# Kernel optimization log

Measured on AMD Instinct MI355X. Metric: run time of the kernel, lower is better.

## Reference

```python
import jax, jax.numpy as jnp
import numpy as np

# --- dims (match init_kwargs) ---
B, IN_DIM, OUT_DIM, CAUSES_DIM = 4096, 512, 4096, 256
POOL = 2
N_STEPS = 10
GAMMA = 0.1
LR = 0.001  # fixed lr inside _IstaStep
S = int(np.sqrt(OUT_DIM))   # 64: side of the square code map
SP = S // POOL              # 32: pooled side
POOLED_DIM = SP * SP        # 1024: second dim of V (pool path)


def setup_inputs() -> dict:
    key = jax.random.key(0)
    k1, k2, k3 = jax.random.split(key, 3)
    inputs = jax.random.normal(k1, (B, IN_DIM), jnp.float32)
    limit = float(np.sqrt(6.0 / (OUT_DIM + IN_DIM)))  # glorot_uniform for W
    W = jax.random.uniform(k2, (OUT_DIM, IN_DIM), jnp.float32, -limit, limit)
    # pool_flag=True -> V ~ U(0, 1) with shape (causes_dim, pooled_dim)
    V = jax.random.uniform(k3, (CAUSES_DIM, POOLED_DIM), jnp.float32, 0.0, 1.0)
    return {"inputs": inputs, "W": W, "V": V}


def _soft_threshold(x, t):
    # _proxOp: max(x - t, 0) + min(x + t, 0)
    return jnp.maximum(x - t, 0.0) + jnp.minimum(x + t, 0.0)


def reference(inputs, W, V):
    Bn = inputs.shape[0]
    x0 = jnp.zeros((Bn, OUT_DIM), inputs.dtype)
    u0 = jnp.full((Bn, CAUSES_DIM), 0.1, inputs.dtype)   # zeros + 0.1
    rec0 = jnp.zeros((Bn, IN_DIM), inputs.dtype)

    def step(carry, _):
        x, u, _rec = carry
        outputs = x @ W                                   # [B, IN_DIM], linear activation
        # NOTE: original uses (1 + exp(-z)) * 0.5 (not a true sigmoid) — keep faithful
        causes = (1.0 + jnp.exp(-(u @ V))) * 0.5          # [B, POOLED_DIM]
        # nearest-neighbor upsample of the pooled cause map back to the code map
        causes_up = jnp.repeat(
            jnp.repeat(causes.reshape(Bn, SP, SP), POOL, axis=1), POOL, axis=2
        ).reshape(Bn, OUT_DIM)                            # [B, OUT_DIM]
        # T.grad(sum((inputs - x@W)^2), x) = 2 * (x@W - inputs) @ W.T
        grad_x = 2.0 * (outputs - inputs) @ W.T           # [B, OUT_DIM]
        # prior=0 in _get_output, so the _proxInnov branch is dead code
        x_new = jax.lax.stop_gradient(                    # disconnected_grad
            _soft_threshold(x - LR * grad_x, LR * GAMMA * causes_up))
        # 2x2 max pool over the square code map
        x_pool = x_new.reshape(Bn, SP, POOL, SP, POOL).max(axis=(2, 4)).reshape(Bn, POOLED_DIM)
        # T.grad(sum(causes(u) * x_pool * gamma), u): d causes/dz = -0.5*exp(-z)
        dcauses = -0.5 * jnp.exp(-(u @ V))                # [B, POOLED_DIM]
        grad_u = (dcauses * x_pool * GAMMA) @ V.T         # [B, CAUSES_DIM]
        u_new = jax.lax.stop_gradient(
            _soft_threshold(u - LR * grad_u, LR * GAMMA / 10.0))
        return (x_new, u_new, outputs), None

    (x, u, rec), _ = jax.lax.scan(step, (x0, u0, rec0), None, length=N_STEPS)
    # return_mode='rec': reconstruction computed in the last step (from x_{T-1})
    return rec
```

## Files before the change

kernel.cpp:

```cpp
#include <hip/hip_runtime.h>
#include <math.h>


#define NB 4096
#define IN_DIM 512
#define OUT_DIM 4096
#define CAUSES_DIM 256
#define POOLED_DIM 1024

typedef __attribute__((ext_vector_type(8))) short short8;
typedef __attribute__((ext_vector_type(4))) float f32x4;

static constexpr float LR = 0.001f;
static constexpr float GAMMA = 0.1f;

enum { EP_R = 0, EP_OUT, EP_UUP };

__device__ __forceinline__ float softthr(float v, float t) {
    return fmaxf(v - t, 0.0f) + fminf(v + t, 0.0f);
}
__device__ __forceinline__ unsigned short f2bf(float f) {
    unsigned int u = __builtin_bit_cast(unsigned int, f);
    u = (u + 0x7fffu + ((u >> 16) & 1u)) >> 16;
    return (unsigned short)u;
}
__device__ __forceinline__ float bf2f(unsigned short h) {
    return __builtin_bit_cast(float, (unsigned int)h << 16);
}
__device__ __forceinline__ void gload_lds16(const unsigned short* g, unsigned short* l) {
    __builtin_amdgcn_global_load_lds(
        (const __attribute__((address_space(1))) void*)g,
        (__attribute__((address_space(3))) void*)l, 16, 0, 0);
}

template<int ROWS, int K>
__device__ __forceinline__ void stage_tile(const unsigned short* __restrict__ g,
                                           unsigned short* l, int row0, int k0, int t)
{
#pragma unroll
    for (int j = 0; j < ROWS / 32; j++) {
        const int idx = j * 256 + t;
        const int row = idx >> 3;
        const int sl  = (idx & 7) ^ (row & 7);
        gload_lds16(g + (size_t)(row0 + row) * K + k0 + sl * 8,
                    l + (size_t)(idx & ~63) * 8);
    }
}

template<int BM, int BN, int N, int K, int EP>
__device__ void gemm_core(unsigned short* lds, int bid,
                          const unsigned short* __restrict__ A,
                          const unsigned short* __restrict__ B,
                          const float* __restrict__ auxf,
                          void* __restrict__ out0, void* __restrict__ out1)
{
    constexpr int WM = BM / 2, WN = BN / 2;
    constexpr int FM = WM / 16, FN = WN / 16;
    constexpr int NK = K / 64, NX = N / BN;
    constexpr int NWG = (NB / BM) * NX;
    constexpr int TILE = (BM + BN) * 64;
    unsigned short* A0 = lds;
    unsigned short* B0 = lds + BM * 64;
    unsigned short* A1 = lds + TILE;
    unsigned short* B1 = lds + TILE + BM * 64;

    const int t    = threadIdx.x;
    const int lane = t & 63, wid = t >> 6;
    const int l15  = lane & 15, l7 = lane & 7, g = lane >> 4;
    const int work = ((bid & 7) * (NWG / 8)) + (bid >> 3);
    const int bn = work % NX, bm = work / NX;
    const int m0 = bm * BM, n0 = bn * BN;
    const int wm0 = (wid >> 1) * WM, wn0 = (wid & 1) * WN;

    f32x4 acc[FM][FN];
#pragma unroll
    for (int fi = 0; fi < FM; fi++)
#pragma unroll
        for (int fj = 0; fj < FN; fj++) acc[fi][fj] = (f32x4){0.f, 0.f, 0.f, 0.f};

    auto compute = [&](const unsigned short* As, const unsigned short* Bs) {
#pragma unroll
        for (int ks = 0; ks < 2; ks++) {
            const int so = (((ks * 4) + g) ^ l7) * 8;
            short8 af[FM], bfv[FN];
#pragma unroll
            for (int fi = 0; fi < FM; fi++)
                af[fi] = *(const short8*)&As[(wm0 + fi * 16 + l15) * 64 + so];
#pragma unroll
            for (int fj = 0; fj < FN; fj++)
                bfv[fj] = *(const short8*)&Bs[(wn0 + fj * 16 + l15) * 64 + so];
#pragma unroll
            for (int fi = 0; fi < FM; fi++)
#pragma unroll
                for (int fj = 0; fj < FN; fj++)
                    acc[fi][fj] = __builtin_amdgcn_mfma_f32_16x16x32_bf16(
                        af[fi], bfv[fj], acc[fi][fj], 0, 0, 0);
        }
    };

    stage_tile<BM, K>(A, A0, m0, 0, t);
    stage_tile<BN, K>(B, B0, n0, 0, t);
    __syncthreads();
#pragma unroll 1
    for (int kt = 0; kt < NK; kt += 2) {
        stage_tile<BM, K>(A, A1, m0, (kt + 1) * 64, t);
        stage_tile<BN, K>(B, B1, n0, (kt + 1) * 64, t);
        compute(A0, B0);
        __syncthreads();
        if (kt + 2 < NK) {
            stage_tile<BM, K>(A, A0, m0, (kt + 2) * 64, t);
            stage_tile<BN, K>(B, B0, n0, (kt + 2) * 64, t);
        }
        compute(A1, B1);
        __syncthreads();
    }

#pragma unroll
    for (int fi = 0; fi < FM; fi++) {
#pragma unroll
        for (int fj = 0; fj < FN; fj++) {
#pragma unroll
            for (int r = 0; r < 4; r++) {
                const int row = m0 + wm0 + fi * 16 + g * 4 + r;
                const int col = n0 + wn0 + fj * 16 + l15;
                const float v = acc[fi][fj][r];
                if (EP == EP_R) {
                    ((unsigned short*)out0)[(size_t)row * N + col] =
                        f2bf(v - auxf[(size_t)row * N + col]);
                } else if (EP == EP_OUT) {
                    ((float*)out0)[(size_t)row * N + col] = v;
                } else {
                    float* up = (float*)out0;
                    const size_t idx = (size_t)row * CAUSES_DIM + col;
                    const float uv = softthr(up[idx] - LR * v, LR * GAMMA * 0.1f);
                    up[idx] = uv;
                    ((unsigned short*)out1)[idx] = f2bf(uv);
                }
            }
        }
    }
}

template<bool POOLF>
__global__ __launch_bounds__(256)
void xupc_kernel(const unsigned short* __restrict__ Rbf,
                 const unsigned short* __restrict__ Wbf,
                 const unsigned short* __restrict__ ubf,
                 const unsigned short* __restrict__ VTbf,
                 unsigned short* __restrict__ xbf,
                 unsigned short* __restrict__ gbf)
{
    constexpr int BM = 128, BN = 128, K = IN_DIM, NK = K / 64;
    constexpr int NX = OUT_DIM / BN, NWG = (NB / BM) * NX;
    constexpr int TILE = (BM + BN) * 64;
    __shared__ unsigned short lds[2 * TILE];
    unsigned short* A0 = lds;
    unsigned short* B0 = lds + BM * 64;
    unsigned short* A1 = lds + TILE;
    unsigned short* B1 = lds + TILE + BM * 64;
    unsigned* czdc = (unsigned*)(lds + 2 * TILE - 8192);
    unsigned short* xs = lds;

    const int t    = threadIdx.x;
    const int lane = t & 63, wid = t >> 6;
    const int l15  = lane & 15, l7 = lane & 7, g = lane >> 4;
    const int work = ((blockIdx.x & 7) * (NWG / 8)) + (blockIdx.x >> 3);
    const int bn = work % NX, bm = work / NX;
    const int m0 = bm * BM, n0 = bn * BN;
    const int wm0 = (wid >> 1) * 64, wn0 = (wid & 1) * 64;

    f32x4 acc[4][4];
#pragma unroll
    for (int fi = 0; fi < 4; fi++)
#pragma unroll
        for (int fj = 0; fj < 4; fj++) acc[fi][fj] = (f32x4){0.f, 0.f, 0.f, 0.f};

    auto compute = [&](const unsigned short* As, const unsigned short* Bs) {
#pragma unroll
        for (int ks = 0; ks < 2; ks++) {
            const int so = (((ks * 4) + g) ^ l7) * 8;
            short8 af[4], bfv[4];
#pragma unroll
            for (int fi = 0; fi < 4; fi++)
                af[fi] = *(const short8*)&As[(wm0 + fi * 16 + l15) * 64 + so];
#pragma unroll
            for (int fj = 0; fj < 4; fj++)
                bfv[fj] = *(const short8*)&Bs[(wn0 + fj * 16 + l15) * 64 + so];
#pragma unroll
            for (int fi = 0; fi < 4; fi++)
#pragma unroll
                for (int fj = 0; fj < 4; fj++)
                    acc[fi][fj] = __builtin_amdgcn_mfma_f32_16x16x32_bf16(
                        af[fi], bfv[fj], acc[fi][fj], 0, 0, 0);
        }
    };

    stage_tile<BM, K>(Rbf, A0, m0, 0, t);
    stage_tile<BN, K>(Wbf, B0, n0, 0, t);
    __syncthreads();
#pragma unroll 1
    for (int kt = 0; kt < NK; kt += 2) {
        stage_tile<BM, K>(Rbf, A1, m0, (kt + 1) * 64, t);
        stage_tile<BN, K>(Wbf, B1, n0, (kt + 1) * 64, t);
        compute(A0, B0);
        __syncthreads();
        if (kt + 2 < NK) {
            stage_tile<BM, K>(Rbf, A0, m0, (kt + 2) * 64, t);
            stage_tile<BN, K>(Wbf, B0, n0, (kt + 2) * 64, t);
        }
        compute(A1, B1);
        __syncthreads();
    }

    f32x4 zacc[4];
#pragma unroll
    for (int fi = 0; fi < 4; fi++) zacc[fi] = (f32x4){0.f, 0.f, 0.f, 0.f};
    const int vrow0 = bn * 32;
    auto zcomp = [&](const unsigned short* As, const unsigned short* Bs) {
#pragma unroll
        for (int ks = 0; ks < 2; ks++) {
            const int so = (((ks * 4) + g) ^ l7) * 8;
            short8 bfv = *(const short8*)&Bs[((wid & 1) * 16 + l15) * 64 + so];
#pragma unroll
            for (int fi = 0; fi < 4; fi++) {
                short8 af = *(const short8*)&As[((wid >> 1) * 64 + fi * 16 + l15) * 64 + so];
                zacc[fi] = __builtin_amdgcn_mfma_f32_16x16x32_bf16(af, bfv, zacc[fi], 0, 0, 0);
            }
        }
    };
    stage_tile<128, CAUSES_DIM>(ubf, A0, m0, 0, t);
    stage_tile<32, CAUSES_DIM>(VTbf, B0, vrow0, 0, t);
    __syncthreads();
    stage_tile<128, CAUSES_DIM>(ubf, A1, m0, 64, t);
    stage_tile<32, CAUSES_DIM>(VTbf, B1, vrow0, 64, t);
    zcomp(A0, B0);
    __syncthreads();
    stage_tile<128, CAUSES_DIM>(ubf, A0, m0, 128, t);
    stage_tile<32, CAUSES_DIM>(VTbf, B0, vrow0, 128, t);
    zcomp(A1, B1);
    __syncthreads();
    stage_tile<128, CAUSES_DIM>(ubf, A1, m0, 192, t);
    stage_tile<32, CAUSES_DIM>(VTbf, B1, vrow0, 192, t);
    zcomp(A0, B0);
    __syncthreads();
    zcomp(A1, B1);
    __syncthreads();

#pragma unroll
    for (int fi = 0; fi < 4; fi++) {
#pragma unroll
        for (int r = 0; r < 4; r++) {
            const int zrow = (wid >> 1) * 64 + fi * 16 + g * 4 + r;
            const int zcol = (wid & 1) * 16 + l15;
            const float e = expf(-zacc[fi][r]);
            czdc[zrow * 32 + zcol] =
                (unsigned)f2bf(0.5f + 0.5f * e) | ((unsigned)f2bf(-0.5f * e) << 16);
        }
    }
    __syncthreads();

#pragma unroll
    for (int fi = 0; fi < 4; fi++) {
#pragma unroll
        for (int fj = 0; fj < 4; fj++) {
#pragma unroll
            for (int r = 0; r < 4; r++) {
                const int rloc = wm0 + fi * 16 + g * 4 + r;
                const int cloc = wn0 + fj * 16 + l15;
                const int pl = (cloc & 63) >> 1;
                const float cz = bf2f((unsigned short)(czdc[rloc * 32 + pl] & 0xffffu));
                const size_t idx = (size_t)(m0 + rloc) * OUT_DIM + n0 + cloc;
                const float xv = softthr(bf2f(xbf[idx]) - 2.0f * LR * acc[fi][fj][r],
                                         LR * GAMMA * cz);
                const unsigned short xq = f2bf(xv);
                xbf[idx] = xq;
                if (POOLF) xs[rloc * 130 + cloc] = xq;
            }
        }
    }

    if (POOLF) {
        __syncthreads();
        const int p = t & 31;
        const int rbase = (t >> 5) * 16;
#pragma unroll
        for (int i = 0; i < 16; i++) {
            const int prow = rbase + i;
            const unsigned short* xr = &xs[prow * 130 + 2 * p];
            const float mx = fmaxf(fmaxf(bf2f(xr[0]), bf2f(xr[1])),
                                   fmaxf(bf2f(xr[64]), bf2f(xr[65])));
            const float dcv = bf2f((unsigned short)(czdc[prow * 32 + p] >> 16));
            gbf[(size_t)(m0 + prow) * POOLED_DIM + bn * 32 + p] = f2bf(dcv * mx * GAMMA);
        }
    }
}

__global__ __launch_bounds__(256)
void h_uup_r_kernel(const unsigned short* __restrict__ gbf,
                    const unsigned short* __restrict__ Vbf,
                    float* __restrict__ u, unsigned short* __restrict__ ubf,
                    const unsigned short* __restrict__ xbf,
                    const unsigned short* __restrict__ WTbf,
                    const float* __restrict__ inputs,
                    unsigned short* __restrict__ Rbf)
{
    __shared__ unsigned short lds[24576];
    if (blockIdx.x < 256) {
        gemm_core<128, 64, IN_DIM, OUT_DIM, EP_R>(
            lds, blockIdx.x, xbf, WTbf, inputs, Rbf, nullptr);
    } else {
        gemm_core<64, 64, CAUSES_DIM, POOLED_DIM, EP_UUP>(
            lds, blockIdx.x - 256, gbf, Vbf, nullptr, u, ubf);
    }
}

__global__ __launch_bounds__(256)
void out_kernel(const unsigned short* __restrict__ xbf,
                const unsigned short* __restrict__ WTbf,
                float* __restrict__ out)
{
    __shared__ unsigned short lds[24576];
    gemm_core<128, 64, IN_DIM, OUT_DIM, EP_OUT>(
        lds, blockIdx.x, xbf, WTbf, nullptr, out, nullptr);
}

__global__ void cast_bf16_k(const float* __restrict__ in, unsigned short* __restrict__ out,
                            int n4, int neg)
{
    const int i = blockIdx.x * 256 + threadIdx.x;
    if (i >= n4) return;
    float4 v = ((const float4*)in)[i];
    if (neg) { v.x = -v.x; v.y = -v.y; v.z = -v.z; v.w = -v.w; }
    union { unsigned short s[4]; unsigned long long u; } p;
    p.s[0] = f2bf(v.x); p.s[1] = f2bf(v.y); p.s[2] = f2bf(v.z); p.s[3] = f2bf(v.w);
    ((unsigned long long*)out)[i] = p.u;
}

__global__ __launch_bounds__(256)
void transpose_cast_k(const float* __restrict__ in, unsigned short* __restrict__ out,
                      int R, int C)
{
    __shared__ float tile[32][33];
    const int bx = blockIdx.x * 32, by = blockIdx.y * 32;
    const int tx = threadIdx.x % 32, ty = threadIdx.x / 32;
#pragma unroll
    for (int i = 0; i < 32; i += 8)
        tile[ty + i][tx] = in[(size_t)(by + ty + i) * C + bx + tx];
    __syncthreads();
#pragma unroll
    for (int i = 0; i < 32; i += 8)
        out[(size_t)(bx + ty + i) * R + by + tx] = f2bf(tile[tx][ty + i]);
}

__global__ void fill_zero_u16(unsigned short* __restrict__ p, size_t n8) {
    for (size_t i = (size_t)blockIdx.x * 256 + threadIdx.x; i < n8;
         i += (size_t)gridDim.x * 256)
        ((ulonglong2*)p)[i] = (ulonglong2){0ull, 0ull};
}

__global__ void fill_u_k(float* __restrict__ u, unsigned short* __restrict__ ubf, int n) {
    const int i = blockIdx.x * 256 + threadIdx.x;
    if (i >= n) return;
    u[i] = 0.1f;
    ubf[i] = f2bf(0.1f);
}

extern "C" void kernel_launch(void* const* d_in, const int* in_sizes, int n_in,
                              void* d_out, int out_size, void* d_ws, size_t ws_size,
                              hipStream_t stream)
{
    const float* inputs = (const float*)d_in[0];
    const float* W      = (const float*)d_in[1];
    const float* V      = (const float*)d_in[2];
    float* out = (float*)d_out;

    char* w = (char*)d_ws;
    unsigned short* xbf  = (unsigned short*)w; w += (size_t)NB * OUT_DIM * 2;
    unsigned short* Rbf  = (unsigned short*)w; w += (size_t)NB * IN_DIM * 2;
    unsigned short* gbf  = (unsigned short*)w; w += (size_t)NB * POOLED_DIM * 2;
    float*          u    = (float*)w;          w += (size_t)NB * CAUSES_DIM * 4;
    unsigned short* ubf  = (unsigned short*)w; w += (size_t)NB * CAUSES_DIM * 2;
    unsigned short* Wbf  = (unsigned short*)w; w += (size_t)OUT_DIM * IN_DIM * 2;
    unsigned short* WTbf = (unsigned short*)w; w += (size_t)OUT_DIM * IN_DIM * 2;
    unsigned short* Vbf  = (unsigned short*)w; w += (size_t)CAUSES_DIM * POOLED_DIM * 2;
    unsigned short* VTbf = (unsigned short*)w;

    cast_bf16_k<<<OUT_DIM * IN_DIM / 4 / 256, 256, 0, stream>>>(W, Wbf, OUT_DIM * IN_DIM / 4, 0);
    cast_bf16_k<<<CAUSES_DIM * POOLED_DIM / 4 / 256, 256, 0, stream>>>(V, Vbf, CAUSES_DIM * POOLED_DIM / 4, 0);
    transpose_cast_k<<<dim3(IN_DIM / 32, OUT_DIM / 32), 256, 0, stream>>>(W, WTbf, OUT_DIM, IN_DIM);
    transpose_cast_k<<<dim3(POOLED_DIM / 32, CAUSES_DIM / 32), 256, 0, stream>>>(V, VTbf, CAUSES_DIM, POOLED_DIM);
    fill_zero_u16<<<2048, 256, 0, stream>>>(xbf, (size_t)NB * OUT_DIM / 8);
    fill_u_k<<<NB * CAUSES_DIM / 256, 256, 0, stream>>>(u, ubf, NB * CAUSES_DIM);
    cast_bf16_k<<<NB * IN_DIM / 4 / 256, 256, 0, stream>>>(inputs, Rbf, NB * IN_DIM / 4, 1);

    for (int t = 0; t < 8; t++) {
        xupc_kernel<true><<<1024, 256, 0, stream>>>(Rbf, Wbf, ubf, VTbf, xbf, gbf);
        h_uup_r_kernel<<<512, 256, 0, stream>>>(gbf, Vbf, u, ubf, xbf, WTbf, inputs, Rbf);
    }
    xupc_kernel<false><<<1024, 256, 0, stream>>>(Rbf, Wbf, ubf, VTbf, xbf, gbf);
    out_kernel<<<256, 256, 0, stream>>>(xbf, WTbf, out);
}
```

Before: 795.2 us.

## Use triple-buffered K pipeline, smaller x-update tiles, and fused weight prep

Replaces the double-buffered GEMM K-loop with a shared three-stage pipeline that waits on vmcnt counts, so global-to-LDS loads overlap more with MFMA compute. The x-update kernel moves to 64x128 tiles, doubling the grid to 2048 blocks. The cause GEMM now reuses the same pipelined loop. A FIRST template variant skips reading the zero x buffer and drops the zero-fill kernel. Weight casts and transposes are fused into one prep kernel. The extra buffer stage raises LDS use per block, which may reduce occupancy.

Measured after the change: 849.0 us. 1.07x slower.

```diff
diff --git a/kernel.cpp b/kernel.cpp
--- a/kernel.cpp
+++ b/kernel.cpp
@@ -47,6 +47,65 @@
     }
 }
 
+template<int BM, int BN, int K>
+__device__ __forceinline__ void kloop(unsigned short* lds,
+    const unsigned short* __restrict__ A, const unsigned short* __restrict__ B,
+    int m0, int n0, f32x4 (&acc)[BM / 32][BN / 32])
+{
+    constexpr int FM = BM / 32, FN = BN / 32;
+    constexpr int NK = K / 64, ST = (BM + BN) * 64, L = (BM + BN) / 32;
+    static_assert(NK >= 3, "pipeline needs >=3 K-tiles");
+    const int t = threadIdx.x;
+    const int lane = t & 63, wid = t >> 6;
+    const int l15 = lane & 15, l7 = lane & 7, g = lane >> 4;
+    const int wm0 = (wid >> 1) * (BM / 2), wn0 = (wid & 1) * (BN / 2);
+
+    auto stage = [&](int s, int b) {
+        stage_tile<BM, K>(A, lds + b * ST, m0, s * 64, t);
+        stage_tile<BN, K>(B, lds + b * ST + BM * 64, n0, s * 64, t);
+    };
+    auto comp = [&](int b) {
+        const unsigned short* As = lds + b * ST;
+        const unsigned short* Bs = lds + b * ST + BM * 64;
+#pragma unroll
+        for (int ks = 0; ks < 2; ks++) {
+            const int so = (((ks * 4) + g) ^ l7) * 8;
+            short8 af[FM], bfv[FN];
+#pragma unroll
+            for (int fi = 0; fi < FM; fi++)
+                af[fi] = *(const short8*)&As[(wm0 + fi * 16 + l15) * 64 + so];
+#pragma unroll
+            for (int fj = 0; fj < FN; fj++)
+                bfv[fj] = *(const short8*)&Bs[(wn0 + fj * 16 + l15) * 64 + so];
+#pragma unroll
+            for (int fi = 0; fi < FM; fi++)
+#pragma unroll
+                for (int fj = 0; fj < FN; fj++)
+                    acc[fi][fj] = __builtin_amdgcn_mfma_f32_16x16x32_bf16(
+                        af[fi], bfv[fj], acc[fi][fj], 0, 0, 0);
+        }
+    };
+
+    stage(0, 0); stage(1, 1); stage(2, 2);
+    int b = 0;
+#pragma unroll 1
+    for (int i = 0; i < NK - 2; ++i) {
+        asm volatile("s_waitcnt vmcnt(%0)" :: "n"(2 * L) : "memory");
+        __builtin_amdgcn_s_barrier();
+        comp(b);
+        __builtin_amdgcn_s_barrier();
+        if (i + 3 < NK) stage(i + 3, b);
+        b = (b == 2) ? 0 : b + 1;
+    }
+    asm volatile("s_waitcnt vmcnt(%0)" :: "n"(L) : "memory");
+    __builtin_amdgcn_s_barrier();
+    comp(b);
+    b = (b == 2) ? 0 : b + 1;
+    asm volatile("s_waitcnt vmcnt(0)" ::: "memory");
+    __builtin_amdgcn_s_barrier();
+    comp(b);
+}
+
 template<int BM, int BN, int N, int K, int EP>
 __device__ void gemm_core(unsigned short* lds, int bid,
                           const unsigned short* __restrict__ A,
@@ -54,23 +113,14 @@
                           const float* __restrict__ auxf,
                           void* __restrict__ out0, void* __restrict__ out1)
 {
-    constexpr int WM = BM / 2, WN = BN / 2;
-    constexpr int FM = WM / 16, FN = WN / 16;
-    constexpr int NK = K / 64, NX = N / BN;
-    constexpr int NWG = (NB / BM) * NX;
-    constexpr int TILE = (BM + BN) * 64;
-    unsigned short* A0 = lds;
-    unsigned short* B0 = lds + BM * 64;
-    unsigned short* A1 = lds + TILE;
-    unsigned short* B1 = lds + TILE + BM * 64;
-
-    const int t    = threadIdx.x;
-    const int lane = t & 63, wid = t >> 6;
-    const int l15  = lane & 15, l7 = lane & 7, g = lane >> 4;
+    constexpr int FM = BM / 32, FN = BN / 32;
+    constexpr int NX = N / BN, NWG = (NB / BM) * NX;
+    const int t = threadIdx.x, lane = t & 63, wid = t >> 6;
+    const int l15 = lane & 15, g = lane >> 4;
     const int work = ((bid & 7) * (NWG / 8)) + (bid >> 3);
     const int bn = work % NX, bm = work / NX;
     const int m0 = bm * BM, n0 = bn * BN;
-    const int wm0 = (wid >> 1) * WM, wn0 = (wid & 1) * WN;
+    const int wm0 = (wid >> 1) * (BM / 2), wn0 = (wid & 1) * (BN / 2);
 
     f32x4 acc[FM][FN];
 #pragma unroll
@@ -78,42 +128,7 @@
 #pragma unroll
         for (int fj = 0; fj < FN; fj++) acc[fi][fj] = (f32x4){0.f, 0.f, 0.f, 0.f};
 
-    auto compute = [&](const unsigned short* As, const unsigned short* Bs) {
-#pragma unroll
-        for (int ks = 0; ks < 2; ks++) {
-            const int so = (((ks * 4) + g) ^ l7) * 8;
-            short8 af[FM], bfv[FN];
-#pragma unroll
-            for (int fi = 0; fi < FM; fi++)
-                af[fi] = *(const short8*)&As[(wm0 + fi * 16 + l15) * 64 + so];
-#pragma unroll
-            for (int fj = 0; fj < FN; fj++)
-                bfv[fj] = *(const short8*)&Bs[(wn0 + fj * 16 + l15) * 64 + so];
-#pragma unroll
-            for (int fi = 0; fi < FM; fi++)
-#pragma unroll
-                for (int fj = 0; fj < FN; fj++)
-                    acc[fi][fj] = __builtin_amdgcn_mfma_f32_16x16x32_bf16(
-                        af[fi], bfv[fj], acc[fi][fj], 0, 0, 0);
-        }
-    };
-
-    stage_tile<BM, K>(A, A0, m0, 0, t);
-    stage_tile<BN, K>(B, B0, n0, 0, t);
-    __syncthreads();
-#pragma unroll 1
-    for (int kt = 0; kt < NK; kt += 2) {
-        stage_tile<BM, K>(A, A1, m0, (kt + 1) * 64, t);
-        stage_tile<BN, K>(B, B1, n0, (kt + 1) * 64, t);
-        compute(A0, B0);
-        __syncthreads();
-        if (kt + 2 < NK) {
-            stage_tile<BM, K>(A, A0, m0, (kt + 2) * 64, t);
-            stage_tile<BN, K>(B, B0, n0, (kt + 2) * 64, t);
-        }
-        compute(A1, B1);
-        __syncthreads();
-    }
+    kloop<BM, BN, K>(lds, A, B, m0, n0, acc);
 
 #pragma unroll
     for (int fi = 0; fi < FM; fi++) {
@@ -141,7 +156,7 @@
     }
 }
 
-template<bool POOLF>
+template<bool FIRST, bool POOLF>
 __global__ __launch_bounds__(256)
 void xupc_kernel(const unsigned short* __restrict__ Rbf,
                  const unsigned short* __restrict__ Wbf,
@@ -150,117 +165,50 @@
                  unsigned short* __restrict__ xbf,
                  unsigned short* __restrict__ gbf)
 {
-    constexpr int BM = 128, BN = 128, K = IN_DIM, NK = K / 64;
-    constexpr int NX = OUT_DIM / BN, NWG = (NB / BM) * NX;
-    constexpr int TILE = (BM + BN) * 64;
-    __shared__ unsigned short lds[2 * TILE];
-    unsigned short* A0 = lds;
-    unsigned short* B0 = lds + BM * 64;
-    unsigned short* A1 = lds + TILE;
-    unsigned short* B1 = lds + TILE + BM * 64;
-    unsigned* czdc = (unsigned*)(lds + 2 * TILE - 8192);
+    constexpr int BM = 64, BN = 128;
+    constexpr int NX = OUT_DIM / BN;
+    constexpr int NWG = (NB / BM) * NX;
+    __shared__ unsigned short lds[3 * (BM + BN) * 64 + 4096];
+    unsigned* czdc = (unsigned*)(lds + 3 * (BM + BN) * 64);
     unsigned short* xs = lds;
 
-    const int t    = threadIdx.x;
-    const int lane = t & 63, wid = t >> 6;
-    const int l15  = lane & 15, l7 = lane & 7, g = lane >> 4;
+    const int t = threadIdx.x, lane = t & 63, wid = t >> 6;
+    const int l15 = lane & 15, g = lane >> 4;
     const int work = ((blockIdx.x & 7) * (NWG / 8)) + (blockIdx.x >> 3);
     const int bn = work % NX, bm = work / NX;
     const int m0 = bm * BM, n0 = bn * BN;
-    const int wm0 = (wid >> 1) * 64, wn0 = (wid & 1) * 64;
-
-    f32x4 acc[4][4];
-#pragma unroll
-    for (int fi = 0; fi < 4; fi++)
+    const int wm0 = (wid >> 1) * 32, wn0 = (wid & 1) * 64;
+
+    f32x4 acc[2][4];
+#pragma unroll
+    for (int fi = 0; fi < 2; fi++)
 #pragma unroll
         for (int fj = 0; fj < 4; fj++) acc[fi][fj] = (f32x4){0.f, 0.f, 0.f, 0.f};
-
-    auto compute = [&](const unsigned short* As, const unsigned short* Bs) {
-#pragma unroll
-        for (int ks = 0; ks < 2; ks++) {
-            const int so = (((ks * 4) + g) ^ l7) * 8;
-            short8 af[4], bfv[4];
-#pragma unroll
-            for (int fi = 0; fi < 4; fi++)
-                af[fi] = *(const short8*)&As[(wm0 + fi * 16 + l15) * 64 + so];
-#pragma unroll
-            for (int fj = 0; fj < 4; fj++)
-                bfv[fj] = *(const short8*)&Bs[(wn0 + fj * 16 + l15) * 64 + so];
-#pragma unroll
-            for (int fi = 0; fi < 4; fi++)
-#pragma unroll
-                for (int fj = 0; fj < 4; fj++)
-                    acc[fi][fj] = __builtin_amdgcn_mfma_f32_16x16x32_bf16(
-                        af[fi], bfv[fj], acc[fi][fj], 0, 0, 0);
-        }
-    };
-
-    stage_tile<BM, K>(Rbf, A0, m0, 0, t);
-    stage_tile<BN, K>(Wbf, B0, n0, 0, t);
+    kloop<64, 128, IN_DIM>(lds, Rbf, Wbf, m0, n0, acc);
     __syncthreads();
-#pragma unroll 1
-    for (int kt = 0; kt < NK; kt += 2) {
-        stage_tile<BM, K>(Rbf, A1, m0, (kt + 1) * 64, t);
-        stage_tile<BN, K>(Wbf, B1, n0, (kt + 1) * 64, t);
-        compute(A0, B0);
-        __syncthreads();
-        if (kt + 2 < NK) {
-            stage_tile<BM, K>(Rbf, A0, m0, (kt + 2) * 64, t);
-            stage_tile<BN, K>(Wbf, B0, n0, (kt + 2) * 64, t);
-        }
-        compute(A1, B1);
-        __syncthreads();
-    }
-
-    f32x4 zacc[4];
-#pragma unroll
-    for (int fi = 0; fi < 4; fi++) zacc[fi] = (f32x4){0.f, 0.f, 0.f, 0.f};
-    const int vrow0 = bn * 32;
-    auto zcomp = [&](const unsigned short* As, const unsigned short* Bs) {
-#pragma unroll
-        for (int ks = 0; ks < 2; ks++) {
-            const int so = (((ks * 4) + g) ^ l7) * 8;
-            short8 bfv = *(const short8*)&Bs[((wid & 1) * 16 + l15) * 64 + so];
-#pragma unroll
-            for (int fi = 0; fi < 4; fi++) {
-                short8 af = *(const short8*)&As[((wid >> 1) * 64 + fi * 16 + l15) * 64 + so];
-                zacc[fi] = __builtin_amdgcn_mfma_f32_16x16x32_bf16(af, bfv, zacc[fi], 0, 0, 0);
+
+    f32x4 zacc[2][1];
+    zacc[0][0] = (f32x4){0.f, 0.f, 0.f, 0.f};
+    zacc[1][0] = (f32x4){0.f, 0.f, 0.f, 0.f};
+    kloop<64, 32, CAUSES_DIM>(lds, ubf, VTbf, m0, bn * 32, zacc);
+
+    {
+        const int zc = (wid & 1) * 16 + l15;
+#pragma unroll
+        for (int fi = 0; fi < 2; fi++) {
+#pragma unroll
+            for (int r = 0; r < 4; r++) {
+                const int zr = (wid >> 1) * 32 + fi * 16 + g * 4 + r;
+                const float e = expf(-zacc[fi][0][r]);
+                czdc[zr * 32 + zc] =
+                    (unsigned)f2bf(0.5f + 0.5f * e) | ((unsigned)f2bf(-0.5f * e) << 16);
             }
         }
-    };
-    stage_tile<128, CAUSES_DIM>(ubf, A0, m0, 0, t);
-    stage_tile<32, CAUSES_DIM>(VTbf, B0, vrow0, 0, t);
+    }
     __syncthreads();
-    stage_tile<128, CAUSES_DIM>(ubf, A1, m0, 64, t);
-    stage_tile<32, CAUSES_DIM>(VTbf, B1, vrow0, 64, t);
-    zcomp(A0, B0);
-    __syncthreads();
-    stage_tile<128, CAUSES_DIM>(ubf, A0, m0, 128, t);
-    stage_tile<32, CAUSES_DIM>(VTbf, B0, vrow0, 128, t);
-    zcomp(A1, B1);
-    __syncthreads();
-    stage_tile<128, CAUSES_DIM>(ubf, A1, m0, 192, t);
-    stage_tile<32, CAUSES_DIM>(VTbf, B1, vrow0, 192, t);
-    zcomp(A0, B0);
-    __syncthreads();
-    zcomp(A1, B1);
-    __syncthreads();
-
-#pragma unroll
-    for (int fi = 0; fi < 4; fi++) {
-#pragma unroll
-        for (int r = 0; r < 4; r++) {
-            const int zrow = (wid >> 1) * 64 + fi * 16 + g * 4 + r;
-            const int zcol = (wid & 1) * 16 + l15;
-            const float e = expf(-zacc[fi][r]);
-            czdc[zrow * 32 + zcol] =
-                (unsigned)f2bf(0.5f + 0.5f * e) | ((unsigned)f2bf(-0.5f * e) << 16);
-        }
-    }
-    __syncthreads();
-
-#pragma unroll
-    for (int fi = 0; fi < 4; fi++) {
+
+#pragma unroll
+    for (int fi = 0; fi < 2; fi++) {
 #pragma unroll
         for (int fj = 0; fj < 4; fj++) {
 #pragma unroll
@@ -270,7 +218,8 @@
                 const int pl = (cloc & 63) >> 1;
                 const float cz = bf2f((unsigned short)(czdc[rloc * 32 + pl] & 0xffffu));
                 const size_t idx = (size_t)(m0 + rloc) * OUT_DIM + n0 + cloc;
-                const float xv = softthr(bf2f(xbf[idx]) - 2.0f * LR * acc[fi][fj][r],
+                const float xold = FIRST ? 0.0f : bf2f(xbf[idx]);
+                const float xv = softthr(xold - 2.0f * LR * acc[fi][fj][r],
                                          LR * GAMMA * cz);
                 const unsigned short xq = f2bf(xv);
                 xbf[idx] = xq;
@@ -282,9 +231,9 @@
     if (POOLF) {
         __syncthreads();
         const int p = t & 31;
-        const int rbase = (t >> 5) * 16;
-#pragma unroll
-        for (int i = 0; i < 16; i++) {
+        const int rbase = (t >> 5) * 8;
+#pragma unroll
+        for (int i = 0; i < 8; i++) {
             const int prow = rbase + i;
             const unsigned short* xr = &xs[prow * 130 + 2 * p];
             const float mx = fmaxf(fmaxf(bf2f(xr[0]), bf2f(xr[1])),
@@ -304,7 +253,7 @@
                     const float* __restrict__ inputs,
                     unsigned short* __restrict__ Rbf)
 {
-    __shared__ unsigned short lds[24576];
+    __shared__ unsigned short lds[3 * (128 + 64) * 64];
     if (blockIdx.x < 256) {
         gemm_core<128, 64, IN_DIM, OUT_DIM, EP_R>(
             lds, blockIdx.x, xbf, WTbf, inputs, Rbf, nullptr);
@@ -319,43 +268,39 @@
                 const unsigned short* __restrict__ WTbf,
                 float* __restrict__ out)
 {
-    __shared__ unsigned short lds[24576];
+    __shared__ unsigned short lds[3 * (128 + 64) * 64];
     gemm_core<128, 64, IN_DIM, OUT_DIM, EP_OUT>(
         lds, blockIdx.x, xbf, WTbf, nullptr, out, nullptr);
 }
 
-__global__ void cast_bf16_k(const float* __restrict__ in, unsigned short* __restrict__ out,
-                            int n4, int neg)
+__global__ __launch_bounds__(256)
+void prep_k(const float* __restrict__ in, unsigned short* __restrict__ direct,
+            unsigned short* __restrict__ transp, int R, int C)
+{
+    __shared__ float tile[32][33];
+    const int bx = blockIdx.x * 32, by = blockIdx.y * 32;
+    const int tx = threadIdx.x % 32, ty = threadIdx.x / 32;
+#pragma unroll
+    for (int i = 0; i < 32; i += 8) {
+        const float v = in[(size_t)(by + ty + i) * C + bx + tx];
+        tile[ty + i][tx] = v;
+        direct[(size_t)(by + ty + i) * C + bx + tx] = f2bf(v);
+    }
+    __syncthreads();
+#pragma unroll
+    for (int i = 0; i < 32; i += 8)
+        transp[(size_t)(bx + ty + i) * R + by + tx] = f2bf(tile[tx][ty + i]);
+}
+
+__global__ void negcast_k(const float* __restrict__ in, unsigned short* __restrict__ out,
+                          int n4)
 {
     const int i = blockIdx.x * 256 + threadIdx.x;
     if (i >= n4) return;
     float4 v = ((const float4*)in)[i];
-    if (neg) { v.x = -v.x; v.y = -v.y; v.z = -v.z; v.w = -v.w; }
     union { unsigned short s[4]; unsigned long long u; } p;
-    p.s[0] = f2bf(v.x); p.s[1] = f2bf(v.y); p.s[2] = f2bf(v.z); p.s[3] = f2bf(v.w);
+    p.s[0] = f2bf(-v.x); p.s[1] = f2bf(-v.y); p.s[2] = f2bf(-v.z); p.s[3] = f2bf(-v.w);
     ((unsigned long long*)out)[i] = p.u;
-}
-
-__global__ __launch_bounds__(256)
-void transpose_cast_k(const float* __restrict__ in, unsigned short* __restrict__ out,
-                      int R, int C)
-{
-    __shared__ float tile[32][33];
-    const int bx = blockIdx.x * 32, by = blockIdx.y * 32;
-    const int tx = threadIdx.x % 32, ty = threadIdx.x / 32;
-#pragma unroll
-    for (int i = 0; i < 32; i += 8)
-        tile[ty + i][tx] = in[(size_t)(by + ty + i) * C + bx + tx];
-    __syncthreads();
-#pragma unroll
-    for (int i = 0; i < 32; i += 8)
-        out[(size_t)(bx + ty + i) * R + by + tx] = f2bf(tile[tx][ty + i]);
-}
-
-__global__ void fill_zero_u16(unsigned short* __restrict__ p, size_t n8) {
-    for (size_t i = (size_t)blockIdx.x * 256 + threadIdx.x; i < n8;
-         i += (size_t)gridDim.x * 256)
-        ((ulonglong2*)p)[i] = (ulonglong2){0ull, 0ull};
 }
 
 __global__ void fill_u_k(float* __restrict__ u, unsigned short* __restrict__ ubf, int n) {
@@ -385,18 +330,17 @@
     unsigned short* Vbf  = (unsigned short*)w; w += (size_t)CAUSES_DIM * POOLED_DIM * 2;
     unsigned short* VTbf = (unsigned short*)w;
 
-    cast_bf16_k<<<OUT_DIM * IN_DIM / 4 / 256, 256, 0, stream>>>(W, Wbf, OUT_DIM * IN_DIM / 4, 0);
-    cast_bf16_k<<<CAUSES_DIM * POOLED_DIM / 4 / 256, 256, 0, stream>>>(V, Vbf, CAUSES_DIM * POOLED_DIM / 4, 0);
-    transpose_cast_k<<<dim3(IN_DIM / 32, OUT_DIM / 32), 256, 0, stream>>>(W, WTbf, OUT_DIM, IN_DIM);
-    transpose_cast_k<<<dim3(POOLED_DIM / 32, CAUSES_DIM / 32), 256, 0, stream>>>(V, VTbf, CAUSES_DIM, POOLED_DIM);
-    fill_zero_u16<<<2048, 256, 0, stream>>>(xbf, (size_t)NB * OUT_DIM / 8);
+    prep_k<<<dim3(IN_DIM / 32, OUT_DIM / 32), 256, 0, stream>>>(W, Wbf, WTbf, OUT_DIM, IN_DIM);
+    prep_k<<<dim3(POOLED_DIM / 32, CAUSES_DIM / 32), 256, 0, stream>>>(V, Vbf, VTbf, CAUSES_DIM, POOLED_DIM);
     fill_u_k<<<NB * CAUSES_DIM / 256, 256, 0, stream>>>(u, ubf, NB * CAUSES_DIM);
-    cast_bf16_k<<<NB * IN_DIM / 4 / 256, 256, 0, stream>>>(inputs, Rbf, NB * IN_DIM / 4, 1);
-
-    for (int t = 0; t < 8; t++) {
-        xupc_kernel<true><<<1024, 256, 0, stream>>>(Rbf, Wbf, ubf, VTbf, xbf, gbf);
+    negcast_k<<<NB * IN_DIM / 4 / 256, 256, 0, stream>>>(inputs, Rbf, NB * IN_DIM / 4);
+
+    xupc_kernel<true, true><<<2048, 256, 0, stream>>>(Rbf, Wbf, ubf, VTbf, xbf, gbf);
+    h_uup_r_kernel<<<512, 256, 0, stream>>>(gbf, Vbf, u, ubf, xbf, WTbf, inputs, Rbf);
+    for (int t = 1; t < 8; t++) {
+        xupc_kernel<false, true><<<2048, 256, 0, stream>>>(Rbf, Wbf, ubf, VTbf, xbf, gbf);
         h_uup_r_kernel<<<512, 256, 0, stream>>>(gbf, Vbf, u, ubf, xbf, WTbf, inputs, Rbf);
     }
-    xupc_kernel<false><<<1024, 256, 0, stream>>>(Rbf, Wbf, ubf, VTbf, xbf, gbf);
+    xupc_kernel<false, false><<<2048, 256, 0, stream>>>(Rbf, Wbf, ubf, VTbf, xbf, gbf);
     out_kernel<<<256, 256, 0, stream>>>(xbf, WTbf, out);
 }
```
